# Kernel optimization log

Hardware: AMD Instinct MI355X
Metric: run time of the kernel (lower is better)

Reference implementation:

```python
import jax, jax.numpy as jnp
import numpy as np

NUM_ORI = 4
VM_R, VM_RG = 10.0, 15.0
B_INH, G_INH = 1.5, 1.0
VM_W, VM_W2 = 0.1, 0.4
VM_WG, VM_W2G = 0.2, 0.4
BORDER_K = 11   # int(10*1.1)=11, already odd
GROUP_K = 23    # int(15*1.5)=22 -> +1 to make odd


def create_von_mises(size, r0, theta0, centered, w, w2):
    x = np.arange(size) - size / 2
    y = -(np.arange(size) - size / 2)
    X, Y = np.meshgrid(x, y)
    if centered:
        X = X + r0 * np.cos(theta0)
        Y = Y + r0 * np.sin(theta0)
    r = np.sqrt(X ** 2 + Y ** 2)
    th = np.arctan2(Y, X)
    # np.i0 == scipy.special.iv(0, .) for real args (I0 is even)
    return np.exp(r0 * w * np.cos(th - theta0)) / np.i0(w2 * (r - r0))


def make_filters():
    borders, groups = [], []
    for ori in np.arange(0.0, 180.0, 180.0 / NUM_ORI):
        a = ori * np.pi / 180.0
        b = (ori + 180.0) * np.pi / 180.0
        borders.append(create_von_mises(BORDER_K, VM_R, a, True, VM_W, VM_W2))
        borders.append(create_von_mises(BORDER_K, VM_R, b, True, VM_W, VM_W2))
        g1 = create_von_mises(GROUP_K, VM_RG, a, False, VM_W, VM_W2)
        g2 = create_von_mises(GROUP_K, VM_RG, b, False, VM_WG, VM_W2G)
        groups += [g1, g1, g2, g2]
    # only border filters are normalized to [-1, 1] in the original code
    borders = [f / (f.max() / 2.0) - 1.0 for f in borders]
    Wb = np.stack(borders)[:, None].astype(np.float32)   # [2*O, 1, 11, 11]
    Wg = np.stack(groups)[:, None].astype(np.float32)    # [4*O, 1, 23, 23]
    return jnp.asarray(Wb), jnp.asarray(Wg)


def setup_inputs() -> dict:
    key = jax.random.key(0)
    inp = jax.random.uniform(key, (4, 2, 512, 512), dtype=jnp.float32)
    Wb, Wg = make_filters()
    return {"inp": inp, "W_border": Wb, "W_group": Wg}


def _conv(x, w, pad, groups):
    return jax.lax.conv_general_dilated(
        x, w, (1, 1), [(pad, pad), (pad, pad)],
        dimension_numbers=("NCHW", "OIHW", "NCHW"),
        feature_group_count=groups)


def _spike(v):
    # LIF with tau_mem=0.01, zero initial v_mem, single step: alpha=exp(-1/tau)~0,
    # so v_mem = input; spike when v_mem >= threshold (1.0).
    return (v >= 1.0).astype(v.dtype)


def reference(inp, W_border, W_group):
    B, _, H, W = inp.shape
    pad_b = (BORDER_K - 1) // 2
    pad_g = (GROUP_K - 1) // 2
    # border ownership: conv each polarity with the 8 von-Mises filters + LIF
    pos = _spike(_conv(inp[:, 0:1], W_border, pad_b, 1))  # [B, 2*O, H, W]
    neg = _spike(_conv(inp[:, 1:2], W_border, pad_b, 1))
    vmap_ = inp.sum(1)[:, None]                           # [B, 1, H, W]
    pe, po = pos[:, 0::2], pos[:, 1::2]   # even=ori, odd=opposite ori
    ne, no = neg[:, 0::2], neg[:, 1::2]
    b13 = _spike(vmap_ * (pe - no * B_INH)) + _spike(vmap_ * (ne - po * B_INH))
    b24 = _spike(vmap_ * (po - ne * B_INH)) + _spike(vmap_ * (no - pe * B_INH))
    # winner-take-all over orientations
    diff = b13 - b24                                      # [B, O, H, W]
    tp = jnp.abs(diff)
    wta = jax.lax.stop_gradient(
        (tp == tp.max(axis=1, keepdims=True)).astype(inp.dtype))
    b1p = _spike(wta * diff)
    b1n = _spike(-(wta * diff))
    # channel order is ori-major: [t1_o, t2_o, t3_o, t4_o] per orientation
    border = jnp.stack(
        [b1p * b13, b1p * b24 * G_INH, b1n * b24, b1n * b13 * G_INH],
        axis=2).reshape(B, 4 * NUM_ORI, H, W)
    g = _spike(_conv(border, W_group, pad_g, 4 * NUM_ORI))
    g = g.reshape(B, NUM_ORI, 4, H, W)
    return (_spike(g[:, :, 0] - g[:, :, 1])
            + _spike(g[:, :, 2] - g[:, :, 3])).sum(1)     # [B, H, W]
```

## Files before the change

kernel.cpp:

```cpp
#include <hip/hip_runtime.h>

#define HH 512
#define WW 512
#define NB 4

#define K1 11
#define PAD1 5
#define T1X 32
#define T1Y 32
#define IN1 42
#define S1B 44

__global__ __launch_bounds__(256, 4) void stage1_kernel(
    const float* __restrict__ inp, const float* __restrict__ Wb,
    unsigned char* __restrict__ border)
{
    __shared__ __align__(16) float s0[IN1 * S1B];
    __shared__ __align__(16) float s1[IN1 * S1B];

    const int b   = blockIdx.z;
    const int tx0 = blockIdx.x * T1X;
    const int ty0 = blockIdx.y * T1Y;
    const float* in0 = inp + ((size_t)b * 2 + 0) * (HH * WW);
    const float* in1 = inp + ((size_t)b * 2 + 1) * (HH * WW);

    for (int i = threadIdx.x; i < IN1 * IN1; i += 256) {
        int iy = i / IN1, ix = i - iy * IN1;
        int gy = ty0 + iy - PAD1, gx = tx0 + ix - PAD1;
        bool ok = (gy >= 0) & (gy < HH) & (gx >= 0) & (gx < WW);
        int idx = gy * WW + gx;
        s0[iy * S1B + ix] = ok ? in0[idx] : 0.f;
        s1[iy * S1B + ix] = ok ? in1[idx] : 0.f;
    }
    __syncthreads();

    const int lx  = threadIdx.x & 7;
    const int ly  = threadIdx.x >> 3;
    const int px0 = lx * 4;
    const int py  = ly;

    float accP[8][4], accN[8][4];
    #pragma unroll
    for (int c = 0; c < 8; c++)
        #pragma unroll
        for (int p = 0; p < 4; p++) { accP[c][p] = 0.f; accN[c][p] = 0.f; }

    #pragma unroll 1
    for (int ky = 0; ky < K1; ky++) {
        float a0[14], a1[14];
        const float2* r0 = (const float2*)&s0[(py + ky) * S1B + px0];
        const float2* r1 = (const float2*)&s1[(py + ky) * S1B + px0];
        #pragma unroll
        for (int r = 0; r < 7; r++) {
            *(float2*)&a0[2 * r] = r0[r];
            *(float2*)&a1[2 * r] = r1[r];
        }
        #pragma unroll
        for (int c = 0; c < 8; c++) {
            #pragma unroll
            for (int kx = 0; kx < K1; kx++) {
                const float wv = Wb[c * 121 + ky * 11 + kx];
                #pragma unroll
                for (int p = 0; p < 4; p++) {
                    accP[c][p] = fmaf(a0[kx + p], wv, accP[c][p]);
                    accN[c][p] = fmaf(a1[kx + p], wv, accN[c][p]);
                }
            }
        }
    }

    const int gy  = ty0 + py;
    const int gxb = tx0 + px0;

    float vm[4];
    #pragma unroll
    for (int p = 0; p < 4; p++)
        vm[p] = s0[(py + PAD1) * S1B + px0 + PAD1 + p]
              + s1[(py + PAD1) * S1B + px0 + PAD1 + p];

    float b13[4][4], b24[4][4];
    #pragma unroll
    for (int o = 0; o < 4; o++) {
        #pragma unroll
        for (int p = 0; p < 4; p++) {
            float pe = (accP[2 * o    ][p] >= 1.f) ? 1.f : 0.f;
            float po = (accP[2 * o + 1][p] >= 1.f) ? 1.f : 0.f;
            float ne = (accN[2 * o    ][p] >= 1.f) ? 1.f : 0.f;
            float no = (accN[2 * o + 1][p] >= 1.f) ? 1.f : 0.f;
            float sa = (vm[p] * (pe - 1.5f * no) >= 1.f) ? 1.f : 0.f;
            float sb = (vm[p] * (ne - 1.5f * po) >= 1.f) ? 1.f : 0.f;
            b13[o][p] = sa + sb;
            float sc = (vm[p] * (po - 1.5f * ne) >= 1.f) ? 1.f : 0.f;
            float sd = (vm[p] * (no - 1.5f * pe) >= 1.f) ? 1.f : 0.f;
            b24[o][p] = sc + sd;
        }
    }
    float mxp[4];
    #pragma unroll
    for (int p = 0; p < 4; p++) {
        float m = 0.f;
        #pragma unroll
        for (int o = 0; o < 4; o++) m = fmaxf(m, fabsf(b13[o][p] - b24[o][p]));
        mxp[p] = m;
    }
    #pragma unroll
    for (int o = 0; o < 4; o++) {
        unsigned w0 = 0, w1 = 0, w2 = 0, w3 = 0;
        #pragma unroll
        for (int p = 0; p < 4; p++) {
            float d   = b13[o][p] - b24[o][p];
            float wta = (fabsf(d) == mxp[p]) ? 1.f : 0.f;
            float b1p = (wta * d >= 1.f)    ? 1.f : 0.f;
            float b1n = (-(wta * d) >= 1.f) ? 1.f : 0.f;
            w0 |= (unsigned)(unsigned char)(b1p * b13[o][p]) << (8 * p);
            w1 |= (unsigned)(unsigned char)(b1p * b24[o][p]) << (8 * p);
            w2 |= (unsigned)(unsigned char)(b1n * b24[o][p]) << (8 * p);
            w3 |= (unsigned)(unsigned char)(b1n * b13[o][p]) << (8 * p);
        }
        size_t base = (((size_t)b * 16 + 4 * o) * HH + gy) * WW + gxb;
        *(unsigned*)&border[base]                       = w0;
        *(unsigned*)&border[base + (size_t)HH * WW]     = w1;
        *(unsigned*)&border[base + (size_t)2 * HH * WW] = w2;
        *(unsigned*)&border[base + (size_t)3 * HH * WW] = w3;
    }
}

#define K2 23
#define PAD2 11
#define T2X 32
#define T2Y 512
#define SROW 18
#define R2 534

__device__ __forceinline__ float ubyte_f(unsigned dw, int byi) {
    return (float)((dw >> (8 * byi)) & 0xffu);
}

__device__ __forceinline__ void s2_load(const unsigned* __restrict__ tile,
                                        int trow, int lx, unsigned d[8])
{
    const uint2* tp2 = (const uint2*)&tile[trow * SROW + 2 * lx];
    #pragma unroll
    for (int r2 = 0; r2 < 4; r2++) {
        uint2 v = tp2[r2];
        d[2 * r2] = v.x; d[2 * r2 + 1] = v.y;
    }
}

__device__ __forceinline__ void s2_cvt(const unsigned d[8], float a[31])
{
    #pragma unroll
    for (int j = 1; j <= 30; j++) a[j] = ubyte_f(d[j >> 2], j & 3);
}

__global__ __launch_bounds__(256, 4) void stage2_kernel(
    const unsigned char* __restrict__ border, const float* __restrict__ Wg,
    unsigned char* __restrict__ gsp)
{
    __shared__ unsigned tile[R2 * SROW];

    const int z   = blockIdx.z;
    const int b   = z >> 4;
    const int c   = z & 15;
    const int tx0 = blockIdx.x * T2X;
    const unsigned char* bp = border + ((size_t)b * 16 + c) * (HH * WW);

    for (int i = threadIdx.x; i < R2 * 16; i += 256) {
        int iy = i >> 4, cc = i & 15;
        int gy  = iy - PAD2;
        int gx0 = tx0 - 12 + 4 * cc;
        unsigned u = 0;
        if (((unsigned)gy < HH) & ((unsigned)gx0 < WW))
            u = *(const unsigned*)(bp + (size_t)gy * WW + gx0);
        tile[iy * SROW + cc] = u;
    }
    __syncthreads();

    const int lx = threadIdx.x & 3;
    const int ly = threadIdx.x >> 2;
    const int px = lx * 8;
    const int py = ly * 8;

    float acc[8][8];
    #pragma unroll
    for (int dy = 0; dy < 8; dy++)
        #pragma unroll
        for (int p = 0; p < 8; p++) acc[dy][p] = 0.f;

    const float* wc = Wg + c * (K2 * K2);

    unsigned dc[8];
    s2_load(tile, py + 0, lx, dc);

    #pragma unroll 1
    for (int t = 0; t < 7; t++) {
        float a[31];
        s2_cvt(dc, a);
        s2_load(tile, py + t + 1, lx, dc);
        #pragma unroll
        for (int dy = 0; dy < 8; dy++) {
            if (t - dy >= 0) {
                const float* wr = wc + (t - dy) * K2;
                #pragma unroll
                for (int kx = 0; kx < K2; kx++) {
                    const float wv = wr[kx];
                    #pragma unroll
                    for (int p = 0; p < 8; p++)
                        acc[dy][p] = fmaf(a[p + kx + 1], wv, acc[dy][p]);
                }
            }
        }
    }

    #pragma unroll 1
    for (int t = 7; t < 23; t++) {
        float a[31];
        s2_cvt(dc, a);
        s2_load(tile, py + t + 1, lx, dc);
        const float* w0 = wc + t * K2;
        #pragma unroll
        for (int kx = 0; kx < K2; kx++) {
            float wv[8];
            #pragma unroll
            for (int d = 0; d < 8; d++) wv[d] = w0[kx - 23 * d];
            #pragma unroll
            for (int p = 0; p < 8; p++) {
                const float av = a[p + kx + 1];
                #pragma unroll
                for (int d = 0; d < 8; d++)
                    acc[d][p] = fmaf(av, wv[d], acc[d][p]);
            }
        }
    }

    #pragma unroll 1
    for (int t = 23; t < 29; t++) {
        float a[31];
        s2_cvt(dc, a);
        s2_load(tile, py + t + 1, lx, dc);
        #pragma unroll
        for (int dy = 0; dy < 8; dy++) {
            if (t - dy < K2) {
                const float* wr = wc + (t - dy) * K2;
                #pragma unroll
                for (int kx = 0; kx < K2; kx++) {
                    const float wv = wr[kx];
                    #pragma unroll
                    for (int p = 0; p < 8; p++)
                        acc[dy][p] = fmaf(a[p + kx + 1], wv, acc[dy][p]);
                }
            }
        }
    }
    {
        float a[31];
        s2_cvt(dc, a);
        const float* wr = wc + 22 * K2;
        #pragma unroll
        for (int kx = 0; kx < K2; kx++) {
            const float wv = wr[kx];
            #pragma unroll
            for (int p = 0; p < 8; p++)
                acc[7][p] = fmaf(a[p + kx + 1], wv, acc[7][p]);
        }
    }

    const int ox = tx0 + px;
    unsigned char* gp = gsp + ((size_t)b * 16 + c) * (HH * WW);
    #pragma unroll
    for (int dy = 0; dy < 8; dy++) {
        const int oy = py + dy;
        unsigned lo = 0, hi = 0;
        #pragma unroll
        for (int p = 0; p < 4; p++) lo |= (acc[dy][p]     >= 1.f ? 1u : 0u) << (8 * p);
        #pragma unroll
        for (int p = 0; p < 4; p++) hi |= (acc[dy][p + 4] >= 1.f ? 1u : 0u) << (8 * p);
        uint2 v; v.x = lo; v.y = hi;
        *(uint2*)&gp[(size_t)oy * WW + ox] = v;
    }
}

__global__ __launch_bounds__(256) void combine_kernel(
    const unsigned char* __restrict__ gsp, float* __restrict__ out)
{
    const int idx = blockIdx.x * 256 + threadIdx.x;
    const int b = idx >> 16;
    const int r = idx & 65535;
    const unsigned* g = (const unsigned*)gsp;
    const int pb = b * 16;
    unsigned s = 0;
    #pragma unroll
    for (int o = 0; o < 4; o++) {
        unsigned g0 = g[(size_t)(pb + 4 * o + 0) * 65536 + r];
        unsigned g1 = g[(size_t)(pb + 4 * o + 1) * 65536 + r];
        unsigned g2 = g[(size_t)(pb + 4 * o + 2) * 65536 + r];
        unsigned g3 = g[(size_t)(pb + 4 * o + 3) * 65536 + r];
        s += ((g0 & ~g1) & 0x01010101u) + ((g2 & ~g3) & 0x01010101u);
    }
    float4 f;
    f.x = (float)(s & 255u);
    f.y = (float)((s >> 8) & 255u);
    f.z = (float)((s >> 16) & 255u);
    f.w = (float)(s >> 24);
    ((float4*)out)[idx] = f;
}

extern "C" void kernel_launch(void* const* d_in, const int* in_sizes, int n_in,
                              void* d_out, int out_size, void* d_ws, size_t ws_size,
                              hipStream_t stream)
{
    const float* inp = (const float*)d_in[0];
    const float* Wb  = (const float*)d_in[1];
    const float* Wg  = (const float*)d_in[2];
    unsigned char* border = (unsigned char*)d_ws;
    unsigned char* gsp    = border + (size_t)NB * 16 * HH * WW;
    float* out = (float*)d_out;

    dim3 blk(256);
    dim3 g1(WW / T1X, HH / T1Y, NB);
    stage1_kernel<<<g1, blk, 0, stream>>>(inp, Wb, border);
    dim3 g2(WW / T2X, 1, NB * 16);
    stage2_kernel<<<g2, blk, 0, stream>>>(border, Wg, gsp);
    dim3 g3((NB * HH * WW / 4) / 256);
    combine_kernel<<<g3, blk, 0, stream>>>(gsp, out);
}
```

Baseline: 264.3 us.

## Use packed FP32 FMA with a zero-padded weight table in group convolution

Adds a prep kernel that expands the 23x23 group filters into a zero-padded [channel][30 rows][23][8 dy] table, written to scratch space at an offset inside the output buffer. The stage-2 convolution then runs a single uniform 30-iteration row loop with no boundary branches. Accumulators are packed pairs of output rows, so each multiply-add becomes a two-wide packed FMA. This is meant to halve the FMA issue count and simplify control flow. In exchange it does about 30% more multiply-adds on padded zeros, adds one kernel launch, and borrows output memory as temporary storage until the combine kernel overwrites it.

```diff
diff --git a/kernel.cpp b/kernel.cpp
--- a/kernel.cpp
+++ b/kernel.cpp
@@ -3,6 +3,25 @@
 #define HH 512
 #define WW 512
 #define NB 4
+
+typedef float v2f __attribute__((ext_vector_type(2)));
+
+#define WG3_ELEMS 88320
+
+__global__ __launch_bounds__(256) void prep_kernel(
+    const float* __restrict__ Wg, float* __restrict__ Wg3)
+{
+    const int e = blockIdx.x * 256 + threadIdx.x;
+    if (e >= WG3_ELEMS) return;
+    const int d  = e & 7;
+    const int r  = e >> 3;
+    const int kx = r % 23;
+    const int r2 = r / 23;
+    const int t  = r2 % 30;
+    const int c  = r2 / 30;
+    const int ky = t - d;
+    Wg3[e] = (ky >= 0 && ky < 23) ? Wg[c * 529 + ky * 23 + kx] : 0.f;
+}
 
 #define K1 11
 #define PAD1 5
@@ -147,14 +166,8 @@
     }
 }
 
-__device__ __forceinline__ void s2_cvt(const unsigned d[8], float a[31])
-{
-    #pragma unroll
-    for (int j = 1; j <= 30; j++) a[j] = ubyte_f(d[j >> 2], j & 3);
-}
-
 __global__ __launch_bounds__(256, 4) void stage2_kernel(
-    const unsigned char* __restrict__ border, const float* __restrict__ Wg,
+    const unsigned char* __restrict__ border, const float* __restrict__ Wg3,
     unsigned char* __restrict__ gsp)
 {
     __shared__ unsigned tile[R2 * SROW];
@@ -181,87 +194,36 @@
     const int px = lx * 8;
     const int py = ly * 8;
 
-    float acc[8][8];
-    #pragma unroll
-    for (int dy = 0; dy < 8; dy++)
-        #pragma unroll
-        for (int p = 0; p < 8; p++) acc[dy][p] = 0.f;
-
-    const float* wc = Wg + c * (K2 * K2);
+    v2f acc2[4][8];
+    #pragma unroll
+    for (int d2 = 0; d2 < 4; d2++)
+        #pragma unroll
+        for (int p = 0; p < 8; p++) acc2[d2][p] = (v2f){0.f, 0.f};
+
+    const float* wc3 = Wg3 + (size_t)c * (30 * 184);
 
     unsigned dc[8];
     s2_load(tile, py + 0, lx, dc);
 
     #pragma unroll 1
-    for (int t = 0; t < 7; t++) {
-        float a[31];
-        s2_cvt(dc, a);
-        s2_load(tile, py + t + 1, lx, dc);
-        #pragma unroll
-        for (int dy = 0; dy < 8; dy++) {
-            if (t - dy >= 0) {
-                const float* wr = wc + (t - dy) * K2;
-                #pragma unroll
-                for (int kx = 0; kx < K2; kx++) {
-                    const float wv = wr[kx];
-                    #pragma unroll
-                    for (int p = 0; p < 8; p++)
-                        acc[dy][p] = fmaf(a[p + kx + 1], wv, acc[dy][p]);
-                }
-            }
-        }
-    }
-
-    #pragma unroll 1
-    for (int t = 7; t < 23; t++) {
-        float a[31];
-        s2_cvt(dc, a);
-        s2_load(tile, py + t + 1, lx, dc);
-        const float* w0 = wc + t * K2;
+    for (int t = 0; t < 30; t++) {
+        float cv[30];
+        #pragma unroll
+        for (int j = 0; j < 30; j++) cv[j] = ubyte_f(dc[(j + 1) >> 2], (j + 1) & 3);
+        if (t < 29) s2_load(tile, py + t + 1, lx, dc);
+
+        const v2f* wt = (const v2f*)(wc3 + t * 184);
         #pragma unroll
         for (int kx = 0; kx < K2; kx++) {
-            float wv[8];
-            #pragma unroll
-            for (int d = 0; d < 8; d++) wv[d] = w0[kx - 23 * d];
             #pragma unroll
             for (int p = 0; p < 8; p++) {
-                const float av = a[p + kx + 1];
+                const float cs = cv[p + kx];
+                const v2f cb = {cs, cs};
                 #pragma unroll
-                for (int d = 0; d < 8; d++)
-                    acc[d][p] = fmaf(av, wv[d], acc[d][p]);
+                for (int d2 = 0; d2 < 4; d2++)
+                    acc2[d2][p] = __builtin_elementwise_fma(cb, wt[kx * 4 + d2],
+                                                            acc2[d2][p]);
             }
-        }
-    }
-
-    #pragma unroll 1
-    for (int t = 23; t < 29; t++) {
-        float a[31];
-        s2_cvt(dc, a);
-        s2_load(tile, py + t + 1, lx, dc);
-        #pragma unroll
-        for (int dy = 0; dy < 8; dy++) {
-            if (t - dy < K2) {
-                const float* wr = wc + (t - dy) * K2;
-                #pragma unroll
-                for (int kx = 0; kx < K2; kx++) {
-                    const float wv = wr[kx];
-                    #pragma unroll
-                    for (int p = 0; p < 8; p++)
-                        acc[dy][p] = fmaf(a[p + kx + 1], wv, acc[dy][p]);
-                }
-            }
-        }
-    }
-    {
-        float a[31];
-        s2_cvt(dc, a);
-        const float* wr = wc + 22 * K2;
-        #pragma unroll
-        for (int kx = 0; kx < K2; kx++) {
-            const float wv = wr[kx];
-            #pragma unroll
-            for (int p = 0; p < 8; p++)
-                acc[7][p] = fmaf(a[p + kx + 1], wv, acc[7][p]);
         }
     }
 
@@ -272,9 +234,15 @@
         const int oy = py + dy;
         unsigned lo = 0, hi = 0;
         #pragma unroll
-        for (int p = 0; p < 4; p++) lo |= (acc[dy][p]     >= 1.f ? 1u : 0u) << (8 * p);
-        #pragma unroll
-        for (int p = 0; p < 4; p++) hi |= (acc[dy][p + 4] >= 1.f ? 1u : 0u) << (8 * p);
+        for (int p = 0; p < 4; p++) {
+            float av = (dy & 1) ? acc2[dy >> 1][p].y : acc2[dy >> 1][p].x;
+            lo |= (av >= 1.f ? 1u : 0u) << (8 * p);
+        }
+        #pragma unroll
+        for (int p = 0; p < 4; p++) {
+            float av = (dy & 1) ? acc2[dy >> 1][p + 4].y : acc2[dy >> 1][p + 4].x;
+            hi |= (av >= 1.f ? 1u : 0u) << (8 * p);
+        }
         uint2 v; v.x = lo; v.y = hi;
         *(uint2*)&gp[(size_t)oy * WW + ox] = v;
     }
@@ -316,11 +284,14 @@
     unsigned char* gsp    = border + (size_t)NB * 16 * HH * WW;
     float* out = (float*)d_out;
 
+    float* Wg3 = (float*)((char*)d_out + (2u << 20));
+
     dim3 blk(256);
+    prep_kernel<<<dim3((WG3_ELEMS + 255) / 256), blk, 0, stream>>>(Wg, Wg3);
     dim3 g1(WW / T1X, HH / T1Y, NB);
     stage1_kernel<<<g1, blk, 0, stream>>>(inp, Wb, border);
     dim3 g2(WW / T2X, 1, NB * 16);
-    stage2_kernel<<<g2, blk, 0, stream>>>(border, Wg, gsp);
+    stage2_kernel<<<g2, blk, 0, stream>>>(border, Wg3, gsp);
     dim3 g3((NB * HH * WW / 4) / 256);
     combine_kernel<<<g3, blk, 0, stream>>>(gsp, out);
 }
```

New measurement: 307.0 us. +16.2%, slower.
